# Kernel optimization log

Measured on AMD Instinct MI355X. Metric: run time of the kernel, lower is better.

Reference implementation:

```python
import jax, jax.numpy as jnp
import numpy as np

B, V, H, W, CIN, COUT = 2, 4, 256, 256, 64, 64
WINDOW = 1
GAMMA = 0.1


def setup_inputs() -> dict:
    key = jax.random.key(0)
    ks = jax.random.split(key, 6)
    # gaussian positions: x,y in [-1,1], z in [0.5,2.5] so projection masks are nontrivial
    means = jax.random.uniform(ks[0], (B, V, H, W, 3), dtype=jnp.float32)
    means = means * jnp.array([2.0, 2.0, 2.0], jnp.float32) + jnp.array([-1.0, -1.0, 0.5], jnp.float32)
    depths = jax.random.uniform(ks[1], (B, V, H, W, 1, 1), dtype=jnp.float32)
    gs_feats = jax.random.normal(ks[2], (B, V, H, W, CIN), dtype=jnp.float32)
    # normalized intrinsics (ndc in [0,1))
    intr = jnp.array([[0.8, 0.0, 0.5], [0.0, 0.8, 0.5], [0.0, 0.0, 1.0]], jnp.float32)
    intrinsics = jnp.broadcast_to(intr, (B, V, 3, 3))
    # camera-to-world extrinsics: identity rotation, small per-view translations
    t = jax.random.uniform(ks[3], (B, V, 3), minval=-0.2, maxval=0.2, dtype=jnp.float32)
    extrinsics = jnp.broadcast_to(jnp.eye(4, dtype=jnp.float32), (B, V, 4, 4)).at[..., :3, 3].set(t)
    w1 = jax.random.normal(ks[4], (COUT, CIN, 3, 3), dtype=jnp.float32) * 0.05
    b1 = jnp.zeros((COUT,), jnp.float32)
    w2 = jax.random.normal(ks[5], (COUT, COUT, 3, 3), dtype=jnp.float32) * 0.05
    b2 = jnp.zeros((COUT,), jnp.float32)
    return {"means": means, "depths": depths, "gs_feats": gs_feats,
            "intrinsics": intrinsics, "extrinsics": extrinsics,
            "w1": w1, "b1": b1, "w2": w2, "b2": b2}


def _project(points, intr, extr, eps=1e-8):
    # points (b, n, 3) world; extr (b,4,4) cam-to-world; intr (b,3,3) normalized
    w2c = jnp.linalg.inv(extr)
    ph = jnp.concatenate([points, jnp.ones_like(points[..., :1])], axis=-1)  # (b,n,4)
    cam = jnp.einsum('bij,bnj->bni', w2c, ph)[..., :3]
    z = cam[..., 2:3]
    ndc = jnp.einsum('bij,bnj->bni', intr, cam / (z + eps))
    return ndc[..., :2], cam[..., 2] > eps


def _conv3x3(x, w, b):
    y = jax.lax.conv_general_dilated(x, w, (1, 1), 'SAME',
                                     dimension_numbers=('NCHW', 'OIHW', 'NCHW'))
    return y + b[None, :, None, None]


def reference(means, depths, gs_feats, intrinsics, extrinsics, w1, b1, w2, b2):
    b, v, h, w_, c = gs_feats.shape
    hw = h * w_
    feats_flat = gs_feats.reshape(b, v, hw, c)
    pts = means.reshape(b, v, hw, 3)
    outs = []
    for j in range(v):
        acc = feats_flat[:, j]                      # (b, hw, c)
        norm = jnp.ones((b,), gs_feats.dtype)
        for k in range(v):
            if j != k and (k - WINDOW) <= j <= (k + WINDOW):
                ndc, valid_z = _project(pts[:, j], intrinsics[:, k], extrinsics[:, k])
                px = jnp.floor(ndc[..., 0] * w_).astype(jnp.int32)
                py = jnp.floor(ndc[..., 1] * h).astype(jnp.int32)
                mask = ((ndc[..., 0] >= 0) & (ndc[..., 0] < 1) &
                        (ndc[..., 1] >= 0) & (ndc[..., 1] < 1) & valid_z)  # (b,hw)
                idx = jnp.clip(py, 0, h - 1) * w_ + jnp.clip(px, 0, w_ - 1)
                gathered = jnp.take_along_axis(feats_flat[:, k], idx[..., None], axis=1)
                upd = jnp.where(mask[..., None], gathered, jnp.zeros((), gs_feats.dtype))
                scale = GAMMA * mask.sum(-1).astype(gs_feats.dtype) / (h * w_)  # (b,)
                acc = acc + upd * scale[:, None, None]
                norm = norm + scale
        outs.append(acc / norm[:, None, None])
    fused = jnp.stack(outs, axis=1).reshape(b * v, h, w_, c).transpose(0, 3, 1, 2)  # (bv,c,h,w)
    x = _conv3x3(fused, w1, b1)
    x = jax.nn.gelu(x, approximate=False)
    x = _conv3x3(x, w2, b2)
    return x.transpose(0, 2, 3, 1).reshape(b, v, h, w_, -1)
```

## Files before the change

kernel.cpp:

```cpp
#include <hip/hip_runtime.h>
#include <math.h>

#define HW 65536
#define NPAD 258

typedef short bf16x8 __attribute__((ext_vector_type(8)));
typedef float f32x4  __attribute__((ext_vector_type(4)));

#define O_COUNTS 0
#define O_W2C    2048
#define O_WT     4096
#define O_META   151552
#define O_FUSED  3297280
#define O_X1     71458816

#define HROWB   4224
#define HROWSTR 4240
#define HBUF    25440

__device__ __forceinline__ unsigned short f2bf(float f) {
    unsigned int u = __float_as_uint(f);
    u += 0x7FFFu + ((u >> 16) & 1u);
    return (unsigned short)(u >> 16);
}

__device__ __forceinline__ unsigned int cvt_pk_bf16(float lo, float hi) {
    unsigned int r;
    asm("v_cvt_pk_bf16_f32 %0, %1, %2" : "=v"(r) : "v"(lo), "v"(hi));
    return r;
}

__device__ __forceinline__ float gelu_fast(float v) {
    float x  = v * 0.70710678118654752f;
    float ax = fabsf(x);
    float t  = __builtin_amdgcn_rcpf(fmaf(0.3275911f, ax, 1.0f));
    float p  = fmaf(t, 1.061405429f, -1.453152027f);
    p = fmaf(t, p, 1.421413741f);
    p = fmaf(t, p, -0.284496736f);
    p = fmaf(t, p, 0.254829592f);
    p = p * t;
    float e   = __expf(-x * x);
    float era = fmaf(-p, e, 1.0f);
    float er  = copysignf(era, x);
    return 0.5f * v * (1.0f + er);
}

__global__ __launch_bounds__(256) void prep_kernel(
    const float* __restrict__ extr, const float* __restrict__ w1,
    const float* __restrict__ w2, float* __restrict__ w2c,
    unsigned short* __restrict__ wT, unsigned short* __restrict__ fusedP,
    unsigned short* __restrict__ x1P, int* __restrict__ counts)
{
    int tid = blockIdx.x * blockDim.x + threadIdx.x;
    int nth = gridDim.x * blockDim.x;

    if (blockIdx.x == 0) {
        if (threadIdx.x < 8) {
            float a[4][8];
            const float* E = extr + threadIdx.x * 16;
            for (int r = 0; r < 4; r++)
                for (int c = 0; c < 4; c++) {
                    a[r][c] = E[r*4 + c];
                    a[r][4+c] = (r == c) ? 1.0f : 0.0f;
                }
            for (int col = 0; col < 4; col++) {
                int piv = col; float bm = fabsf(a[col][col]);
                for (int r = col+1; r < 4; r++) {
                    float v = fabsf(a[r][col]);
                    if (v > bm) { bm = v; piv = r; }
                }
                if (piv != col)
                    for (int c = 0; c < 8; c++) { float t = a[col][c]; a[col][c] = a[piv][c]; a[piv][c] = t; }
                float f = 1.0f / a[col][col];
                for (int c = 0; c < 8; c++) a[col][c] *= f;
                for (int r = 0; r < 4; r++) if (r != col) {
                    float f2 = a[r][col];
                    for (int c = 0; c < 8; c++) a[r][c] -= f2 * a[col][c];
                }
            }
            float* O = w2c + threadIdx.x * 16;
            for (int r = 0; r < 4; r++)
                for (int c = 0; c < 4; c++) O[r*4+c] = a[r][4+c];
        }
    }

    for (int i = tid; i < 384; i += nth) counts[i] = 0;

    for (int e = tid; e < 73728; e += nth) {
        int t = e;
        int j  = t & 7;  t >>= 3;
        int co = t & 63; t >>= 6;
        int q  = t & 3;  t >>= 2;
        int tap = t % 9; t /= 9;
        int h  = t & 1;  int cv = t >> 1;
        int ci = h*32 + q*8 + j;
        int ky = tap / 3, kx = tap % 3;
        const float* wsrc = cv ? w2 : w1;
        float v = wsrc[((co*64 + ci)*3 + ky)*3 + kx];
        wT[cv*36864 + ((((h*9 + tap)*4 + q)*64 + co)*8 + j)] = f2bf(v);
    }

    for (int u = tid; u < 2*8*1028*8; u += nth) {
        int t = u;
        int ch   = t & 7;    t >>= 3;
        int cell = t % 1028; t /= 1028;
        int n    = t & 7;    int buf = t >> 3;
        int y, x;
        if      (cell < 258) { y = 0;   x = cell; }
        else if (cell < 516) { y = 257; x = cell - 258; }
        else if (cell < 772) { y = cell - 516 + 1; x = 0; }
        else                 { y = cell - 772 + 1; x = 257; }
        unsigned short* p = (buf ? x1P : fusedP) +
            (((size_t)(n*NPAD + y)*NPAD + x)*64 + ch*8);
        *reinterpret_cast<uint4*>(p) = make_uint4(0u, 0u, 0u, 0u);
    }
}

__global__ __launch_bounds__(256) void proj_kernel(
    const float* __restrict__ means, const float* __restrict__ intr,
    const float* __restrict__ w2c, int* __restrict__ meta,
    int* __restrict__ counts)
{
    const int jt[6] = {0,1,1,2,2,3};
    const int kt[6] = {1,0,2,1,3,2};
    int s = blockIdx.y;
    int b = s / 6, p = s % 6;
    int j = jt[p], k = kt[p];
    int i = blockIdx.x * 256 + threadIdx.x;

    __shared__ int bcnt;
    if (threadIdx.x == 0) bcnt = 0;
    __syncthreads();

    const float* mp = means + ((size_t)(b*4 + j)*HW + i)*3;
    float x = mp[0], y = mp[1], z = mp[2];
    const float* M = w2c + (b*4 + k)*16;
    const float* I = intr + (b*4 + k)*9;

    float cx = fmaf(M[2],  z, fmaf(M[1], y, M[0]*x)) + M[3];
    float cy = fmaf(M[6],  z, fmaf(M[5], y, M[4]*x)) + M[7];
    float cz = fmaf(M[10], z, fmaf(M[9], y, M[8]*x)) + M[11];

    bool vz = cz > 1e-8f;
    float zi = cz + 1e-8f;
    float sx = cx / zi, sy = cy / zi, sz = cz / zi;
    float nx = fmaf(I[2], sz, fmaf(I[1], sy, I[0]*sx));
    float ny = fmaf(I[5], sz, fmaf(I[4], sy, I[3]*sx));

    int px = (int)floorf(nx * 256.0f);
    int py = (int)floorf(ny * 256.0f);
    bool mask = (nx >= 0.0f) && (nx < 1.0f) && (ny >= 0.0f) && (ny < 1.0f) && vz;
    int pxc = min(max(px, 0), 255);
    int pyc = min(max(py, 0), 255);
    int idx = pyc*256 + pxc;
    meta[(size_t)s*HW + i] = idx | (mask ? (int)0x80000000 : 0);

    unsigned long long bal = __ballot(mask ? 1 : 0);
    if ((threadIdx.x & 63) == 0)
        atomicAdd(&bcnt, (int)__popcll(bal));
    __syncthreads();
    if (threadIdx.x == 0)
        atomicAdd(counts + s*32, bcnt);
}

__global__ __launch_bounds__(256) void fuse_kernel(
    const float* __restrict__ feats, const int* __restrict__ meta,
    const int* __restrict__ counts, unsigned short* __restrict__ fusedP)
{
    const int nsl[4]    = {1, 2, 2, 1};
    const int slt[4][2] = {{0,0},{1,2},{3,4},{5,5}};
    const int kvw[4][2] = {{1,1},{0,2},{1,3},{2,2}};

    int bj = blockIdx.y;
    int b = bj >> 2, j = bj & 3;
    int pt = blockIdx.x * 16 + (threadIdx.x >> 4);
    int cg = threadIdx.x & 15;

    const float4* fj = reinterpret_cast<const float4*>(
        feats + ((size_t)bj*HW + pt)*64) + cg;
    float4 acc = *fj;
    float norm = 1.0f;
    int ns = nsl[j];
    for (int e = 0; e < 2; e++) {
        if (e < ns) {
            int p = slt[j][e], k = kvw[j][e];
            int s = b*6 + p;
            float scale = 0.1f * (float)counts[s*32] / 65536.0f;
            int mt = meta[(size_t)s*HW + pt];
            if (mt < 0) {
                int idx = mt & 0xFFFF;
                const float4* g = reinterpret_cast<const float4*>(
                    feats + ((size_t)(b*4 + k)*HW + idx)*64) + cg;
                float4 gv = *g;
                acc.x += scale * gv.x; acc.y += scale * gv.y;
                acc.z += scale * gv.z; acc.w += scale * gv.w;
            }
            norm += scale;
        }
    }
    float rn = 1.0f / norm;

    int yy = pt >> 8, xx = pt & 255;
    unsigned short* op = fusedP +
        (((size_t)bj*NPAD + (yy+1))*NPAD + (xx+1))*64 + cg*4;
    uint2 o = make_uint2(cvt_pk_bf16(acc.x*rn, acc.y*rn),
                         cvt_pk_bf16(acc.z*rn, acc.w*rn));
    *reinterpret_cast<uint2*>(op) = o;
}

template<int MODE>
__global__ __launch_bounds__(256) void conv_kernel(
    const unsigned short* __restrict__ in, const unsigned short* __restrict__ wT,
    const float* __restrict__ bias, void* __restrict__ outp)
{
    __shared__ unsigned short smem[2 * HBUF / 2];

    int fid = blockIdx.x;
    int wg  = ((fid & 7) << 8) + (fid >> 3);
    int n   = wg >> 8;
    int rem = wg & 255;
    int y0  = (rem >> 2) << 2;
    int X0  = (rem & 3) << 6;

    int w  = threadIdx.x >> 6;
    int lane = threadIdx.x & 63;
    int m = lane & 15, q = lane >> 4;

    int srcl = ((lane >> 2) * 128) + ((((lane & 3) ^ ((lane >> 3) & 3)) & 3) << 4);
    int tsrcl = 8192 + ((lane >> 2) * 128) + ((lane & 3) << 4);

    int vb[3];
#pragma unroll
    for (int dx = 0; dx < 3; dx++)
        vb[dx] = w*HROWSTR + m*64 + (((q ^ (((m + dx) >> 1) & 3)) & 3) << 4);

    int wvoff = q*1024 + m*16;

    const char* gb00 = (const char*)in +
        (((size_t)(n*NPAD) + y0) * NPAD + X0) * 128;

    auto STAGE = [&](int row128, int h, int buf) {
        const char* gb = gb00 + (size_t)row128 * (NPAD*128) + h*64;
        char* lb = (char*)smem + buf*HBUF;
        for (int ri = w; ri < 6; ri += 4) {
            const char* g = gb + (size_t)ri * (NPAD*128);
            char* l = lb + ri*HROWSTR;
#pragma unroll
            for (int i = 0; i < 4; i++)
                __builtin_amdgcn_global_load_lds(
                    (const __attribute__((address_space(1))) unsigned int*)(g + i*2048 + srcl),
                    (__attribute__((address_space(3))) unsigned int*)(l + i*1024 + (size_t)lane*16),
                    16, 0, 0);
            if (lane < 8)
                __builtin_amdgcn_global_load_lds(
                    (const __attribute__((address_space(1))) unsigned int*)(g + tsrcl),
                    (__attribute__((address_space(3))) unsigned int*)(l + 4096 + (size_t)lane*16),
                    16, 0, 0);
        }
    };

    f32x4 acc[4][4];
    auto ACCZERO = [&]() {
#pragma unroll
        for (int a = 0; a < 4; a++)
#pragma unroll
            for (int bq = 0; bq < 4; bq++)
                acc[a][bq] = (f32x4){0.f, 0.f, 0.f, 0.f};
    };

    auto COMPUTE = [&](int h, int buf) {
        const char* sb = (const char*)smem + buf*HBUF;
        const char* wbase = (const char*)wT + h*36864;
        __builtin_amdgcn_s_setprio(1);
#pragma unroll
        for (int tap = 0; tap < 9; tap++) {
            int dy = tap/3, dx = tap%3;
            const char* wtap = wbase + tap*4096;
            bf16x8 av[4], bv[4];
#pragma unroll
            for (int Mt = 0; Mt < 4; Mt++)
                av[Mt] = *reinterpret_cast<const bf16x8*>(
                    sb + vb[dx] + dy*HROWSTR + Mt*1024 + dx*64);
#pragma unroll
            for (int Nt = 0; Nt < 4; Nt++)
                bv[Nt] = *reinterpret_cast<const bf16x8*>(wtap + wvoff + Nt*256);
#pragma unroll
            for (int Mt = 0; Mt < 4; Mt++)
#pragma unroll
                for (int Nt = 0; Nt < 4; Nt++)
                    acc[Mt][Nt] = __builtin_amdgcn_mfma_f32_16x16x32_bf16(
                        bv[Nt], av[Mt], acc[Mt][Nt], 0, 0, 0);
        }
        __builtin_amdgcn_s_setprio(0);
    };

    auto EPI = [&](int row128) {
        int yout = y0 + row128 + w;
        float4 bsv[4];
#pragma unroll
        for (int Nt = 0; Nt < 4; Nt++)
            bsv[Nt] = *reinterpret_cast<const float4*>(bias + Nt*16 + q*4);
        if (MODE == 1) {
            char* obase = (char*)outp +
                (((size_t)(n*NPAD + yout + 1))*NPAD + (X0 + 1))*128 + m*128 + q*8;
#pragma unroll
            for (int Mt = 0; Mt < 4; Mt++) {
                char* ob = obase + Mt*2048;
#pragma unroll
                for (int Nt = 0; Nt < 4; Nt++) {
                    float v0 = gelu_fast(acc[Mt][Nt][0] + bsv[Nt].x);
                    float v1 = gelu_fast(acc[Mt][Nt][1] + bsv[Nt].y);
                    float v2 = gelu_fast(acc[Mt][Nt][2] + bsv[Nt].z);
                    float v3 = gelu_fast(acc[Mt][Nt][3] + bsv[Nt].w);
                    uint2 pk = make_uint2(cvt_pk_bf16(v0, v1), cvt_pk_bf16(v2, v3));
                    *reinterpret_cast<uint2*>(ob + Nt*32) = pk;
                }
            }
        } else {
            char* obase = (char*)outp +
                (((size_t)(n*256 + yout))*256 + X0)*256 + m*256 + q*16;
#pragma unroll
            for (int Mt = 0; Mt < 4; Mt++) {
                char* ob = obase + Mt*4096;
#pragma unroll
                for (int Nt = 0; Nt < 4; Nt++) {
                    float4 v = make_float4(acc[Mt][Nt][0] + bsv[Nt].x,
                                           acc[Mt][Nt][1] + bsv[Nt].y,
                                           acc[Mt][Nt][2] + bsv[Nt].z,
                                           acc[Mt][Nt][3] + bsv[Nt].w);
                    *reinterpret_cast<float4*>(ob + Nt*64) = v;
                }
            }
        }
    };

    ACCZERO();
    STAGE(0, 0, 0);
    __syncthreads();

    STAGE(0, 1, 1);
    COMPUTE(0, 0);
    __syncthreads();

    STAGE(128, 0, 0);
    COMPUTE(1, 1);
    EPI(0);
    ACCZERO();
    __syncthreads();

    STAGE(128, 1, 1);
    COMPUTE(0, 0);
    __syncthreads();

    COMPUTE(1, 1);
    EPI(128);
}

extern "C" void kernel_launch(void* const* d_in, const int* in_sizes, int n_in,
                              void* d_out, int out_size, void* d_ws, size_t ws_size,
                              hipStream_t stream)
{
    const float* means = (const float*)d_in[0];
    const float* feats = (const float*)d_in[2];
    const float* intr  = (const float*)d_in[3];
    const float* extr  = (const float*)d_in[4];
    const float* w1    = (const float*)d_in[5];
    const float* b1    = (const float*)d_in[6];
    const float* w2    = (const float*)d_in[7];
    const float* b2    = (const float*)d_in[8];

    char* ws = (char*)d_ws;
    int*            counts = (int*)(ws + O_COUNTS);
    float*          w2c    = (float*)(ws + O_W2C);
    unsigned short* wT     = (unsigned short*)(ws + O_WT);
    int*            meta   = (int*)(ws + O_META);
    unsigned short* fusedP = (unsigned short*)(ws + O_FUSED);
    unsigned short* x1P    = (unsigned short*)(ws + O_X1);

    prep_kernel<<<dim3(96), dim3(256), 0, stream>>>(
        extr, w1, w2, w2c, wT, fusedP, x1P, counts);
    proj_kernel<<<dim3(256, 12), dim3(256), 0, stream>>>(
        means, intr, w2c, meta, counts);
    fuse_kernel<<<dim3(4096, 8), dim3(256), 0, stream>>>(
        feats, meta, counts, fusedP);
    conv_kernel<1><<<dim3(1024), dim3(256), 0, stream>>>(
        fusedP, wT, b1, (void*)x1P);
    conv_kernel<2><<<dim3(1024), dim3(256), 0, stream>>>(
        x1P, wT + 36864, b2, d_out);
}
```

Before: 379.9 us.

## Pipeline conv kernel over four row tiles with vmcnt waits instead of syncthreads

Each conv workgroup now processes four 64-row-offset tiles in an unrolled loop, and the grid is halved to 512 blocks. Full __syncthreads are replaced with raw s_barrier plus per-wave s_waitcnt vmcnt counts and sched_barriers. This lets the global-to-LDS loads for the next half-tile overlap the MFMA compute and the epilogue of the current one. The block-to-tile mapping also changes from the swizzled mapping to a simple interleave across images. The hand-tuned vmcnt counts are fragile: a wrong count can produce a race on the double-buffered LDS.

```diff
diff --git a/kernel.cpp b/kernel.cpp
--- a/kernel.cpp
+++ b/kernel.cpp
@@ -17,6 +17,10 @@
 #define HROWB   4224
 #define HROWSTR 4240
 #define HBUF    25440
+
+#define BARRIER() __builtin_amdgcn_s_barrier()
+#define SCHED0()  __builtin_amdgcn_sched_barrier(0)
+#define VMWAIT(N) asm volatile("s_waitcnt vmcnt(" #N ")" ::: "memory")
 
 __device__ __forceinline__ unsigned short f2bf(float f) {
     unsigned int u = __float_as_uint(f);
@@ -216,15 +220,15 @@
     __shared__ unsigned short smem[2 * HBUF / 2];
 
     int fid = blockIdx.x;
-    int wg  = ((fid & 7) << 8) + (fid >> 3);
-    int n   = wg >> 8;
-    int rem = wg & 255;
+    int n   = fid & 7;
+    int rem = fid >> 3;
     int y0  = (rem >> 2) << 2;
     int X0  = (rem & 3) << 6;
 
     int w  = threadIdx.x >> 6;
     int lane = threadIdx.x & 63;
     int m = lane & 15, q = lane >> 4;
+    bool wlo = (w < 2);
 
     int srcl = ((lane >> 2) * 128) + ((((lane & 3) ^ ((lane >> 3) & 3)) & 3) << 4);
     int tsrcl = 8192 + ((lane >> 2) * 128) + ((lane & 3) << 4);
@@ -239,8 +243,8 @@
     const char* gb00 = (const char*)in +
         (((size_t)(n*NPAD) + y0) * NPAD + X0) * 128;
 
-    auto STAGE = [&](int row128, int h, int buf) {
-        const char* gb = gb00 + (size_t)row128 * (NPAD*128) + h*64;
+    auto STAGE = [&](int row64, int h, int buf) {
+        const char* gb = gb00 + (size_t)row64 * (NPAD*128) + h*64;
         char* lb = (char*)smem + buf*HBUF;
         for (int ri = w; ri < 6; ri += 4) {
             const char* g = gb + (size_t)ri * (NPAD*128);
@@ -294,8 +298,8 @@
         __builtin_amdgcn_s_setprio(0);
     };
 
-    auto EPI = [&](int row128) {
-        int yout = y0 + row128 + w;
+    auto EPI = [&](int row64) {
+        int yout = y0 + row64 + w;
         float4 bsv[4];
 #pragma unroll
         for (int Nt = 0; Nt < 4; Nt++)
@@ -334,26 +338,36 @@
         }
     };
 
+    auto WAIT_A = [&]() { if (wlo) { VMWAIT(10); } else { VMWAIT(5);  } SCHED0(); };
+    auto WAIT_B = [&]() { if (wlo) { VMWAIT(26); } else { VMWAIT(21); } SCHED0(); };
+
     ACCZERO();
     STAGE(0, 0, 0);
-    __syncthreads();
-
     STAGE(0, 1, 1);
-    COMPUTE(0, 0);
-    __syncthreads();
-
-    STAGE(128, 0, 0);
-    COMPUTE(1, 1);
-    EPI(0);
-    ACCZERO();
-    __syncthreads();
-
-    STAGE(128, 1, 1);
-    COMPUTE(0, 0);
-    __syncthreads();
-
-    COMPUTE(1, 1);
-    EPI(128);
+    WAIT_A();
+    BARRIER(); SCHED0();
+
+#pragma unroll
+    for (int t = 0; t < 4; t++) {
+        COMPUTE(0, 0);
+        BARRIER(); SCHED0();
+        if (t < 3) STAGE((t+1)*64, 0, 0);
+        if (t == 0)      { WAIT_A(); }
+        else if (t < 3)  { WAIT_B(); }
+        else             { VMWAIT(16); SCHED0(); }
+        BARRIER(); SCHED0();
+        COMPUTE(1, 1);
+        if (t < 3) {
+            BARRIER(); SCHED0();
+            STAGE((t+1)*64, 1, 1);
+        }
+        EPI(t*64);
+        if (t < 3) {
+            ACCZERO();
+            WAIT_B();
+            BARRIER(); SCHED0();
+        }
+    }
 }
 
 extern "C" void kernel_launch(void* const* d_in, const int* in_sizes, int n_in,
@@ -383,8 +397,8 @@
         means, intr, w2c, meta, counts);
     fuse_kernel<<<dim3(4096, 8), dim3(256), 0, stream>>>(
         feats, meta, counts, fusedP);
-    conv_kernel<1><<<dim3(1024), dim3(256), 0, stream>>>(
+    conv_kernel<1><<<dim3(512), dim3(256), 0, stream>>>(
         fusedP, wT, b1, (void*)x1P);
-    conv_kernel<2><<<dim3(1024), dim3(256), 0, stream>>>(
+    conv_kernel<2><<<dim3(512), dim3(256), 0, stream>>>(
         x1P, wT + 36864, b2, d_out);
 }
```

Result: slower. 423.3 us (+11.4%).

## Stage conv halo tiles through registers instead of direct global-to-LDS loads

Applied to the files above, without the earlier changes.

Replaces the global_load_lds staging in the conv kernel with explicit register prefetch (global loads into a uint4 array) issued before each compute phase, then swizzled ds_write into the alternate LDS buffer after compute. Sched barriers keep the loads ahead of the MFMA loop so global latency overlaps compute. It also changes the block-to-tile mapping so consecutive blocks walk across images rather than within one image. This raises register pressure (ten uint4 per thread) and adds LDS write instructions, and the new block order may hurt L2 locality.

```diff
diff --git a/kernel.cpp b/kernel.cpp
--- a/kernel.cpp
+++ b/kernel.cpp
@@ -17,6 +17,8 @@
 #define HROWB   4224
 #define HROWSTR 4240
 #define HBUF    25440
+
+#define SCHED0()  __builtin_amdgcn_sched_barrier(0)
 
 __device__ __forceinline__ unsigned short f2bf(float f) {
     unsigned int u = __float_as_uint(f);
@@ -216,9 +218,8 @@
     __shared__ unsigned short smem[2 * HBUF / 2];
 
     int fid = blockIdx.x;
-    int wg  = ((fid & 7) << 8) + (fid >> 3);
-    int n   = wg >> 8;
-    int rem = wg & 255;
+    int n   = fid & 7;
+    int rem = fid >> 3;
     int y0  = (rem >> 2) << 2;
     int X0  = (rem & 3) << 6;
 
@@ -226,8 +227,9 @@
     int lane = threadIdx.x & 63;
     int m = lane & 15, q = lane >> 4;
 
-    int srcl = ((lane >> 2) * 128) + ((((lane & 3) ^ ((lane >> 3) & 3)) & 3) << 4);
-    int tsrcl = 8192 + ((lane >> 2) * 128) + ((lane & 3) << 4);
+    int gsrc  = ((lane >> 2) * 128) + ((lane & 3) << 4);
+    int gtail = 8192 + gsrc;
+    int wls = ((lane >> 2) * 64) + ((((lane & 3) ^ ((lane >> 3) & 3)) & 3) << 4);
 
     int vb[3];
 #pragma unroll
@@ -239,23 +241,45 @@
     const char* gb00 = (const char*)in +
         (((size_t)(n*NPAD) + y0) * NPAD + X0) * 128;
 
-    auto STAGE = [&](int row128, int h, int buf) {
+    uint4 rg[10];
+
+    auto LOADR = [&](int row128, int h) {
         const char* gb = gb00 + (size_t)row128 * (NPAD*128) + h*64;
+        {
+            const char* g = gb + (size_t)w * (NPAD*128);
+#pragma unroll
+            for (int i = 0; i < 4; i++)
+                rg[i] = *reinterpret_cast<const uint4*>(g + i*2048 + gsrc);
+            if (lane < 8)
+                rg[4] = *reinterpret_cast<const uint4*>(g + gtail);
+        }
+        if (w < 2) {
+            const char* g = gb + (size_t)(w + 4) * (NPAD*128);
+#pragma unroll
+            for (int i = 0; i < 4; i++)
+                rg[5+i] = *reinterpret_cast<const uint4*>(g + i*2048 + gsrc);
+            if (lane < 8)
+                rg[9] = *reinterpret_cast<const uint4*>(g + gtail);
+        }
+    };
+
+    auto WRITER = [&](int buf) {
         char* lb = (char*)smem + buf*HBUF;
-        for (int ri = w; ri < 6; ri += 4) {
-            const char* g = gb + (size_t)ri * (NPAD*128);
-            char* l = lb + ri*HROWSTR;
+        {
+            char* l = lb + w*HROWSTR;
 #pragma unroll
             for (int i = 0; i < 4; i++)
-                __builtin_amdgcn_global_load_lds(
-                    (const __attribute__((address_space(1))) unsigned int*)(g + i*2048 + srcl),
-                    (__attribute__((address_space(3))) unsigned int*)(l + i*1024 + (size_t)lane*16),
-                    16, 0, 0);
+                *reinterpret_cast<uint4*>(l + i*1024 + wls) = rg[i];
             if (lane < 8)
-                __builtin_amdgcn_global_load_lds(
-                    (const __attribute__((address_space(1))) unsigned int*)(g + tsrcl),
-                    (__attribute__((address_space(3))) unsigned int*)(l + 4096 + (size_t)lane*16),
-                    16, 0, 0);
+                *reinterpret_cast<uint4*>(l + 4096 + lane*16) = rg[4];
+        }
+        if (w < 2) {
+            char* l = lb + (w + 4)*HROWSTR;
+#pragma unroll
+            for (int i = 0; i < 4; i++)
+                *reinterpret_cast<uint4*>(l + i*1024 + wls) = rg[5+i];
+            if (lane < 8)
+                *reinterpret_cast<uint4*>(l + 4096 + lane*16) = rg[9];
         }
     };
 
@@ -335,21 +359,25 @@
     };
 
     ACCZERO();
-    STAGE(0, 0, 0);
-    __syncthreads();
-
-    STAGE(0, 1, 1);
+    LOADR(0, 0);
+    WRITER(0);
+    __syncthreads();
+
+    LOADR(0, 1); SCHED0();
     COMPUTE(0, 0);
-    __syncthreads();
-
-    STAGE(128, 0, 0);
+    WRITER(1);
+    __syncthreads();
+
+    LOADR(128, 0); SCHED0();
     COMPUTE(1, 1);
+    WRITER(0);
     EPI(0);
     ACCZERO();
     __syncthreads();
 
-    STAGE(128, 1, 1);
+    LOADR(128, 1); SCHED0();
     COMPUTE(0, 0);
+    WRITER(1);
     __syncthreads();
 
     COMPUTE(1, 1);
```

After: 473.0 us. +24.5%, slower.
